# Optimization experiments

Hardware: AMD Instinct MI355X
Metric: run time of the kernel (lower is better)

Reference implementation:

```python
import jax, jax.numpy as jnp
import numpy as np

ALPHA = 0.9     # projection strength
EPS = 1e-3      # Lyapunov positive-definite regularizer (lyapunov_eps)
B, D, H = 32768, 512, 64


def setup_inputs() -> dict:
    key = jax.random.key(0)
    ks = jax.random.split(key, 8)
    def w(k, shape, fan_in):
        return jax.random.normal(k, shape, jnp.float32) * (1.0 / fan_in) ** 0.5
    return dict(
        x=jax.random.normal(ks[0], (B, D), jnp.float32),
        # dynamics MLP f(x): D -> 64 -> 64 -> D
        W1=w(ks[1], (D, H), D), b1=jnp.zeros((H,), jnp.float32),
        W2=w(ks[2], (H, H), H), b2=jnp.zeros((H,), jnp.float32),
        W3=w(ks[3], (H, D), H), b3=jnp.zeros((D,), jnp.float32),
        # Lyapunov MLP V(z): D -> 64 -> 64 -> 1 (+ eps*||z||^2)
        V1=w(ks[4], (D, H), D), c1=jnp.zeros((H,), jnp.float32),
        V2=w(ks[5], (H, H), H), c2=jnp.zeros((H,), jnp.float32),
        V3=w(ks[6], (H, 1), H), c3=jnp.zeros((1,), jnp.float32),
    )


def reference(x, W1, b1, W2, b2, W3, b3, V1, c1, V2, c2, V3, c3):
    def fnet(xx):  # nominal dynamics: [B,D] -> [B,D]
        h = jax.nn.relu(xx @ W1 + b1)
        h = jax.nn.relu(h @ W2 + b2)
        return h @ W3 + b3

    def vnet(z):  # Lyapunov candidate: [B,D] -> [B]
        h = jax.nn.relu(z @ V1 + c1)
        h = jax.nn.relu(h @ V2 + c2)
        return (h @ V3 + c3)[..., 0] + EPS * jnp.sum(z * z, axis=-1)

    def lyap_sum(xx):
        v = vnet(fnet(xx))
        return jnp.sum(v), v

    # grad_v replicates the in-forward lyapunov.backward(...): dV(f(x))/dx, shape [B,D]
    (_, lyap), grad_v = jax.value_and_grad(lyap_sum, has_aux=True)(x)

    f = fnet(x)                                   # [B, D]
    dot = jnp.sum(grad_v * grad_v, axis=-1)       # bmm(gv, fv): per-sample <grad_v, grad_v>
    denom = jnp.sum(grad_v * grad_v)              # global .pow(2).sum() over all elements
    orth = jax.nn.relu(dot + ALPHA * lyap) / denom  # [B]
    return f - orth[:, None] * grad_v             # diag_embed(orth) @ grad_v
```

## Files before the change

kernel.cpp:

```cpp
#include <hip/hip_runtime.h>

#define ALPHA_C 0.9f
#define EPS_C 1e-3f

typedef unsigned short u16;
typedef __attribute__((ext_vector_type(8))) short short8;
typedef __attribute__((ext_vector_type(4))) float f32x4;
#define MFMA(a, b, c) __builtin_amdgcn_mfma_f32_16x16x32_bf16(a, b, c, 0, 0, 0)

__device__ __forceinline__ u16 f2bf(float f) {
  union { float f; unsigned u; } v; v.f = f;
  unsigned u = v.u;
  u += 0x7FFFu + ((u >> 16) & 1u);
  return (u16)(u >> 16);
}
__device__ __forceinline__ float bf2f(u16 h) {
  union { unsigned u; float f; } v; v.u = ((unsigned)h) << 16;
  return v.f;
}

__global__ __launch_bounds__(256) void k_conv(
    const float* __restrict__ W1, const float* __restrict__ W2, const float* __restrict__ W3,
    const float* __restrict__ V1, const float* __restrict__ V2,
    u16* __restrict__ W1T, u16* __restrict__ W1n, u16* __restrict__ W2T, u16* __restrict__ W2n,
    u16* __restrict__ W3T, u16* __restrict__ W3n, u16* __restrict__ V1T, u16* __restrict__ V1n,
    u16* __restrict__ V2T, u16* __restrict__ V2n) {
  int i = blockIdx.x * 256 + threadIdx.x;
  { float v = W1[i]; int k = i >> 6, j = i & 63; u16 b = f2bf(v); W1n[i] = b; W1T[j * 512 + k] = b; }
  { float v = V1[i]; int k = i >> 6, j = i & 63; u16 b = f2bf(v); V1n[i] = b; V1T[j * 512 + k] = b; }
  { float v = W3[i]; int k = i >> 9, n = i & 511; u16 b = f2bf(v); W3n[i] = b; W3T[n * 64 + k] = b; }
  if (i < 4096) {
    { float v = W2[i]; int k = i >> 6, j = i & 63; u16 b = f2bf(v); W2n[i] = b; W2T[j * 64 + k] = b; }
    { float v = V2[i]; int k = i >> 6, j = i & 63; u16 b = f2bf(v); V2n[i] = b; V2T[j * 64 + k] = b; }
  }
}

__global__ __launch_bounds__(256) void k_h12(
    const float* __restrict__ x, const u16* __restrict__ W1T, const float* __restrict__ b1,
    const u16* __restrict__ W2T, const float* __restrict__ b2,
    u16* __restrict__ H1b, u16* __restrict__ H2b) {
  __shared__ u16 As[64 * 136];
  __shared__ u16 Bs[64 * 136];
  __shared__ u16 W2s[64 * 72];
  __shared__ u16 Hs[64 * 72];
  const int tid = threadIdx.x;
  const int lane = tid & 63, w = tid >> 6, q = lane >> 4, r = lane & 15;
  const int m0 = blockIdx.x * 64;

  #pragma unroll
  for (int c = 0; c < 2; ++c) {
    int idx = c * 256 + tid; int a = idx >> 3, k8 = (idx & 7) * 8;
    *(short8*)&W2s[a * 72 + k8] = *(const short8*)&W2T[a * 64 + k8];
  }

  f32x4 acc[4] = {};
  for (int kc = 0; kc < 4; ++kc) {
    __syncthreads();
    #pragma unroll
    for (int c = 0; c < 8; ++c) {
      int idx = c * 256 + tid; int rr = idx >> 5, k4 = (idx & 31) * 4;
      float4 v = *(const float4*)&x[(size_t)(m0 + rr) * 512 + kc * 128 + k4];
      As[rr * 136 + k4 + 0] = f2bf(v.x);
      As[rr * 136 + k4 + 1] = f2bf(v.y);
      As[rr * 136 + k4 + 2] = f2bf(v.z);
      As[rr * 136 + k4 + 3] = f2bf(v.w);
    }
    #pragma unroll
    for (int c = 0; c < 4; ++c) {
      int idx = c * 256 + tid; int rr = idx >> 4, k8 = (idx & 15) * 8;
      *(short8*)&Bs[rr * 136 + k8] = *(const short8*)&W1T[rr * 512 + kc * 128 + k8];
    }
    __syncthreads();
    #pragma unroll
    for (int ks = 0; ks < 4; ++ks) {
      short8 a = *(const short8*)&As[(w * 16 + r) * 136 + ks * 32 + q * 8];
      #pragma unroll
      for (int t = 0; t < 4; ++t) {
        short8 b = *(const short8*)&Bs[(t * 16 + r) * 136 + ks * 32 + q * 8];
        acc[t] = MFMA(a, b, acc[t]);
      }
    }
  }
  __syncthreads();
  #pragma unroll
  for (int t = 0; t < 4; ++t) {
    int col = t * 16 + r; float bv = b1[col];
    #pragma unroll
    for (int g = 0; g < 4; ++g) {
      float h = acc[t][g] + bv; h = h > 0.f ? h : 0.f;
      Hs[(w * 16 + q * 4 + g) * 72 + col] = f2bf(h);
    }
  }
  __syncthreads();
  #pragma unroll
  for (int c = 0; c < 2; ++c) {
    int idx = c * 256 + tid; int rr = idx >> 3, k8 = (idx & 7) * 8;
    *(short8*)&H1b[(size_t)(m0 + rr) * 64 + k8] = *(const short8*)&Hs[rr * 72 + k8];
  }
  f32x4 acc2[4] = {};
  #pragma unroll
  for (int ks = 0; ks < 2; ++ks) {
    short8 a = *(const short8*)&Hs[(w * 16 + r) * 72 + ks * 32 + q * 8];
    #pragma unroll
    for (int t = 0; t < 4; ++t) {
      short8 b = *(const short8*)&W2s[(t * 16 + r) * 72 + ks * 32 + q * 8];
      acc2[t] = MFMA(a, b, acc2[t]);
    }
  }
  __syncthreads();
  #pragma unroll
  for (int t = 0; t < 4; ++t) {
    int col = t * 16 + r; float bv = b2[col];
    #pragma unroll
    for (int g = 0; g < 4; ++g) {
      float h = acc2[t][g] + bv; h = h > 0.f ? h : 0.f;
      Hs[(w * 16 + q * 4 + g) * 72 + col] = f2bf(h);
    }
  }
  __syncthreads();
  #pragma unroll
  for (int c = 0; c < 2; ++c) {
    int idx = c * 256 + tid; int rr = idx >> 3, k8 = (idx & 7) * 8;
    *(short8*)&H2b[(size_t)(m0 + rr) * 64 + k8] = *(const short8*)&Hs[rr * 72 + k8];
  }
}

__global__ __launch_bounds__(256) void k_fg1s(
    const u16* __restrict__ H2b, const u16* __restrict__ W3T, const float* __restrict__ b3,
    const u16* __restrict__ V1T, const float* __restrict__ c1,
    const u16* __restrict__ V2Tb, const u16* __restrict__ V2nb, const float* __restrict__ c2,
    const float* __restrict__ V3, const float* __restrict__ c3,
    u16* __restrict__ Fb, u16* __restrict__ S2b, float* __restrict__ LYAP) {
  __shared__ u16 H2s[64 * 72];
  __shared__ u16 Bs[128 * 72];
  __shared__ u16 As[64 * 136];
  const int tid = threadIdx.x;
  const int lane = tid & 63, w = tid >> 6, q = lane >> 4, r = lane & 15;
  const int m0 = blockIdx.x * 64;

  #pragma unroll
  for (int c = 0; c < 2; ++c) {
    int idx = c * 256 + tid; int a = idx >> 3, k8 = (idx & 7) * 8;
    *(short8*)&H2s[a * 72 + k8] = *(const short8*)&H2b[(size_t)(m0 + a) * 64 + k8];
  }
  f32x4 g1acc[4] = {};
  float ssq[4] = {0.f, 0.f, 0.f, 0.f};
  for (int nc = 0; nc < 4; ++nc) {
    __syncthreads();
    #pragma unroll
    for (int c = 0; c < 4; ++c) {
      int idx = c * 256 + tid; int nl = idx >> 3, k8 = (idx & 7) * 8;
      *(short8*)&Bs[nl * 72 + k8] = *(const short8*)&W3T[(size_t)(nc * 128 + nl) * 64 + k8];
    }
    __syncthreads();
    f32x4 facc[8] = {};
    #pragma unroll
    for (int ks = 0; ks < 2; ++ks) {
      short8 a = *(const short8*)&H2s[(w * 16 + r) * 72 + ks * 32 + q * 8];
      #pragma unroll
      for (int t = 0; t < 8; ++t) {
        short8 b = *(const short8*)&Bs[(t * 16 + r) * 72 + ks * 32 + q * 8];
        facc[t] = MFMA(a, b, facc[t]);
      }
    }
    #pragma unroll
    for (int t = 0; t < 8; ++t) {
      int colg = nc * 128 + t * 16 + r;
      float bv = b3[colg];
      #pragma unroll
      for (int g = 0; g < 4; ++g) {
        float v = facc[t][g] + bv;
        ssq[g] += v * v;
        As[(w * 16 + q * 4 + g) * 136 + t * 16 + r] = f2bf(v);
      }
    }
    __syncthreads();
    #pragma unroll
    for (int c = 0; c < 4; ++c) {
      int idx = c * 256 + tid; int jj = idx >> 4, k8 = (idx & 15) * 8;
      *(short8*)&Bs[jj * 136 + k8] = *(const short8*)&V1T[(size_t)jj * 512 + nc * 128 + k8];
    }
    __syncthreads();
    #pragma unroll
    for (int ks = 0; ks < 4; ++ks) {
      short8 a = *(const short8*)&As[(w * 16 + r) * 136 + ks * 32 + q * 8];
      #pragma unroll
      for (int t = 0; t < 4; ++t) {
        short8 b = *(const short8*)&Bs[(t * 16 + r) * 136 + ks * 32 + q * 8];
        g1acc[t] = MFMA(a, b, g1acc[t]);
      }
    }
    #pragma unroll
    for (int c = 0; c < 4; ++c) {
      int idx = c * 256 + tid; int rr = idx >> 4, k8 = (idx & 15) * 8;
      *(short8*)&Fb[(size_t)(m0 + rr) * 512 + nc * 128 + k8] = *(const short8*)&As[rr * 136 + k8];
    }
  }
  __syncthreads();
  f32x4 g1v[4];
  #pragma unroll
  for (int t = 0; t < 4; ++t) {
    int col = t * 16 + r; float cv = c1[col];
    #pragma unroll
    for (int g = 0; g < 4; ++g) {
      float v = g1acc[t][g] + cv; v = v > 0.f ? v : 0.f;
      g1v[t][g] = v;
      H2s[(w * 16 + q * 4 + g) * 72 + col] = f2bf(v);
    }
  }
  #pragma unroll
  for (int c = 0; c < 2; ++c) {
    int idx = c * 256 + tid; int a = idx >> 3, k8 = (idx & 7) * 8;
    *(short8*)&Bs[a * 72 + k8] = *(const short8*)&V2Tb[a * 64 + k8];
  }
  __syncthreads();
  f32x4 g2acc[4] = {};
  #pragma unroll
  for (int ks = 0; ks < 2; ++ks) {
    short8 a = *(const short8*)&H2s[(w * 16 + r) * 72 + ks * 32 + q * 8];
    #pragma unroll
    for (int t = 0; t < 4; ++t) {
      short8 b = *(const short8*)&Bs[(t * 16 + r) * 72 + ks * 32 + q * 8];
      g2acc[t] = MFMA(a, b, g2acc[t]);
    }
  }
  __syncthreads();
  float tot[4] = {0.f, 0.f, 0.f, 0.f};
  #pragma unroll
  for (int t = 0; t < 4; ++t) {
    int col = t * 16 + r;
    float c2v = c2[col], v3v = V3[col];
    #pragma unroll
    for (int g = 0; g < 4; ++g) {
      float pre = g2acc[t][g] + c2v;
      float g2 = pre > 0.f ? pre : 0.f;
      float s3 = pre > 0.f ? v3v : 0.f;
      H2s[(w * 16 + q * 4 + g) * 72 + col] = f2bf(s3);
      tot[g] += g2 * v3v;
    }
  }
  #pragma unroll
  for (int c = 0; c < 2; ++c) {
    int idx = c * 256 + tid; int a = idx >> 3, k8 = (idx & 7) * 8;
    *(short8*)&Bs[a * 72 + k8] = *(const short8*)&V2nb[a * 64 + k8];
  }
  __syncthreads();
  f32x4 s2acc[4] = {};
  #pragma unroll
  for (int ks = 0; ks < 2; ++ks) {
    short8 a = *(const short8*)&H2s[(w * 16 + r) * 72 + ks * 32 + q * 8];
    #pragma unroll
    for (int t = 0; t < 4; ++t) {
      short8 b = *(const short8*)&Bs[(t * 16 + r) * 72 + ks * 32 + q * 8];
      s2acc[t] = MFMA(a, b, s2acc[t]);
    }
  }
  #pragma unroll
  for (int t = 0; t < 4; ++t) {
    int col = t * 16 + r;
    #pragma unroll
    for (int g = 0; g < 4; ++g) {
      float sv = g1v[t][g] > 0.f ? s2acc[t][g] : 0.f;
      S2b[(size_t)(m0 + w * 16 + q * 4 + g) * 64 + col] = f2bf(sv);
    }
  }
  float c3v = c3[0];
  #pragma unroll
  for (int g = 0; g < 4; ++g) {
    float s = tot[g] + EPS_C * ssq[g];
    s += __shfl_xor(s, 1); s += __shfl_xor(s, 2); s += __shfl_xor(s, 4); s += __shfl_xor(s, 8);
    if (r == 0) LYAP[m0 + w * 16 + q * 4 + g] = s + c3v;
  }
}

__global__ __launch_bounds__(256) void k_utg(
    const u16* __restrict__ S2b, const u16* __restrict__ V1n, const u16* __restrict__ Fb,
    const u16* __restrict__ W3n, const u16* __restrict__ W2n, const u16* __restrict__ W1n,
    const u16* __restrict__ H1b, const u16* __restrict__ H2b,
    const float* __restrict__ LYAP,
    u16* __restrict__ T2b, float* __restrict__ NUM, float* __restrict__ DP) {
  __shared__ u16 S2s[64 * 72];
  __shared__ u16 Bs[128 * 72];
  __shared__ u16 As[64 * 136];
  __shared__ u16 W2s[64 * 72];
  __shared__ u16 T3s[64 * 72];
  __shared__ float dred[4];
  const int tid = threadIdx.x;
  const int lane = tid & 63, w = tid >> 6, q = lane >> 4, r = lane & 15;
  const int m0 = blockIdx.x * 64;

  #pragma unroll
  for (int c = 0; c < 2; ++c) {
    int idx = c * 256 + tid; int a = idx >> 3, k8 = (idx & 7) * 8;
    *(short8*)&S2s[a * 72 + k8] = *(const short8*)&S2b[(size_t)(m0 + a) * 64 + k8];
    *(short8*)&W2s[a * 72 + k8] = *(const short8*)&W2n[a * 64 + k8];
  }
  f32x4 t3acc[4] = {};
  for (int nc = 0; nc < 4; ++nc) {
    __syncthreads();
    #pragma unroll
    for (int c = 0; c < 4; ++c) {
      int idx = c * 256 + tid; int rr = idx >> 4, k8 = (idx & 15) * 8;
      *(short8*)&As[rr * 136 + k8] = *(const short8*)&Fb[(size_t)(m0 + rr) * 512 + nc * 128 + k8];
    }
    #pragma unroll
    for (int c = 0; c < 4; ++c) {
      int idx = c * 256 + tid; int nl = idx >> 3, k8 = (idx & 7) * 8;
      *(short8*)&Bs[nl * 72 + k8] = *(const short8*)&V1n[(size_t)(nc * 128 + nl) * 64 + k8];
    }
    __syncthreads();
    f32x4 uacc[8] = {};
    #pragma unroll
    for (int ks = 0; ks < 2; ++ks) {
      short8 a = *(const short8*)&S2s[(w * 16 + r) * 72 + ks * 32 + q * 8];
      #pragma unroll
      for (int t = 0; t < 8; ++t) {
        short8 b = *(const short8*)&Bs[(t * 16 + r) * 72 + ks * 32 + q * 8];
        uacc[t] = MFMA(a, b, uacc[t]);
      }
    }
    #pragma unroll
    for (int t = 0; t < 8; ++t) {
      #pragma unroll
      for (int g = 0; g < 4; ++g) {
        int addr = (w * 16 + q * 4 + g) * 136 + t * 16 + r;
        As[addr] = f2bf(uacc[t][g] + 2.f * EPS_C * bf2f(As[addr]));
      }
    }
    __syncthreads();
    #pragma unroll
    for (int c = 0; c < 4; ++c) {
      int idx = c * 256 + tid; int jj = idx >> 4, k8 = (idx & 15) * 8;
      *(short8*)&Bs[jj * 136 + k8] = *(const short8*)&W3n[(size_t)jj * 512 + nc * 128 + k8];
    }
    __syncthreads();
    #pragma unroll
    for (int ks = 0; ks < 4; ++ks) {
      short8 a = *(const short8*)&As[(w * 16 + r) * 136 + ks * 32 + q * 8];
      #pragma unroll
      for (int t = 0; t < 4; ++t) {
        short8 b = *(const short8*)&Bs[(t * 16 + r) * 136 + ks * 32 + q * 8];
        t3acc[t] = MFMA(a, b, t3acc[t]);
      }
    }
  }
  #pragma unroll
  for (int t = 0; t < 4; ++t) {
    int col = t * 16 + r;
    #pragma unroll
    for (int g = 0; g < 4; ++g) {
      int rl = w * 16 + q * 4 + g;
      u16 h2u = H2b[(size_t)(m0 + rl) * 64 + col];
      float v = h2u ? t3acc[t][g] : 0.f;
      T3s[rl * 72 + col] = f2bf(v);
    }
  }
  f32x4 t2acc[4] = {};
  #pragma unroll
  for (int ks = 0; ks < 2; ++ks) {
    short8 a = *(const short8*)&T3s[(w * 16 + r) * 72 + ks * 32 + q * 8];
    #pragma unroll
    for (int t = 0; t < 4; ++t) {
      short8 b = *(const short8*)&W2s[(t * 16 + r) * 72 + ks * 32 + q * 8];
      t2acc[t] = MFMA(a, b, t2acc[t]);
    }
  }
  __syncthreads();
  #pragma unroll
  for (int t = 0; t < 4; ++t) {
    int col = t * 16 + r;
    #pragma unroll
    for (int g = 0; g < 4; ++g) {
      int rl = w * 16 + q * 4 + g;
      u16 h1u = H1b[(size_t)(m0 + rl) * 64 + col];
      u16 tv = h1u ? f2bf(t2acc[t][g]) : 0;
      T2b[(size_t)(m0 + rl) * 64 + col] = tv;
      S2s[rl * 72 + col] = tv;
    }
  }
  float ssq[4] = {0.f, 0.f, 0.f, 0.f};
  for (int nc = 0; nc < 4; ++nc) {
    __syncthreads();
    #pragma unroll
    for (int c = 0; c < 4; ++c) {
      int idx = c * 256 + tid; int nl = idx >> 3, k8 = (idx & 7) * 8;
      *(short8*)&Bs[nl * 72 + k8] = *(const short8*)&W1n[(size_t)(nc * 128 + nl) * 64 + k8];
    }
    __syncthreads();
    f32x4 acc[8] = {};
    #pragma unroll
    for (int ks = 0; ks < 2; ++ks) {
      short8 a = *(const short8*)&S2s[(w * 16 + r) * 72 + ks * 32 + q * 8];
      #pragma unroll
      for (int t = 0; t < 8; ++t) {
        short8 b = *(const short8*)&Bs[(t * 16 + r) * 72 + ks * 32 + q * 8];
        acc[t] = MFMA(a, b, acc[t]);
      }
    }
    #pragma unroll
    for (int t = 0; t < 8; ++t)
      #pragma unroll
      for (int g = 0; g < 4; ++g) ssq[g] += acc[t][g] * acc[t][g];
  }
  float totw = 0.f;
  #pragma unroll
  for (int g = 0; g < 4; ++g) {
    float s = ssq[g];
    s += __shfl_xor(s, 1); s += __shfl_xor(s, 2); s += __shfl_xor(s, 4); s += __shfl_xor(s, 8);
    if (r == 0) {
      int rowg = m0 + w * 16 + q * 4 + g;
      float nm = s + ALPHA_C * LYAP[rowg];
      NUM[rowg] = nm > 0.f ? nm : 0.f;
    }
    s += __shfl_xor(s, 16); s += __shfl_xor(s, 32);
    totw += s;
  }
  if (lane == 0) dred[w] = totw;
  __syncthreads();
  if (tid == 0) atomicAdd(&DP[blockIdx.x & 255], dred[0] + dred[1] + dred[2] + dred[3]);
}

__global__ __launch_bounds__(256) void k_out(
    const u16* __restrict__ T2b, const u16* __restrict__ W1n,
    const u16* __restrict__ Fb, const float* __restrict__ NUM, const float* __restrict__ DP,
    float* __restrict__ out) {
  __shared__ u16 T2s[64 * 72];
  __shared__ u16 Bs[128 * 72];
  __shared__ u16 As[64 * 136];
  __shared__ float red[256];
  const int tid = threadIdx.x;
  const int lane = tid & 63, w = tid >> 6, q = lane >> 4, r = lane & 15;
  const int m0 = blockIdx.x * 64;
  red[tid] = DP[tid];
  #pragma unroll
  for (int c = 0; c < 2; ++c) {
    int idx = c * 256 + tid; int a = idx >> 3, k8 = (idx & 7) * 8;
    *(short8*)&T2s[a * 72 + k8] = *(const short8*)&T2b[(size_t)(m0 + a) * 64 + k8];
  }
  __syncthreads();
  for (int s = 128; s >= 1; s >>= 1) {
    if (tid < s) red[tid] += red[tid + s];
    __syncthreads();
  }
  const float inv_denom = 1.f / red[0];
  float sc[4];
  #pragma unroll
  for (int g = 0; g < 4; ++g) sc[g] = NUM[m0 + w * 16 + q * 4 + g] * inv_denom;
  for (int nc = 0; nc < 4; ++nc) {
    __syncthreads();
    #pragma unroll
    for (int c = 0; c < 4; ++c) {
      int idx = c * 256 + tid; int nl = idx >> 3, k8 = (idx & 7) * 8;
      *(short8*)&Bs[nl * 72 + k8] = *(const short8*)&W1n[(size_t)(nc * 128 + nl) * 64 + k8];
    }
    #pragma unroll
    for (int c = 0; c < 4; ++c) {
      int idx = c * 256 + tid; int rr = idx >> 4, k8 = (idx & 15) * 8;
      *(short8*)&As[rr * 136 + k8] = *(const short8*)&Fb[(size_t)(m0 + rr) * 512 + nc * 128 + k8];
    }
    __syncthreads();
    f32x4 acc[8] = {};
    #pragma unroll
    for (int ks = 0; ks < 2; ++ks) {
      short8 a = *(const short8*)&T2s[(w * 16 + r) * 72 + ks * 32 + q * 8];
      #pragma unroll
      for (int t = 0; t < 8; ++t) {
        short8 b = *(const short8*)&Bs[(t * 16 + r) * 72 + ks * 32 + q * 8];
        acc[t] = MFMA(a, b, acc[t]);
      }
    }
    #pragma unroll
    for (int t = 0; t < 8; ++t) {
      int colg = nc * 128 + t * 16 + r;
      #pragma unroll
      for (int g = 0; g < 4; ++g) {
        int rl = w * 16 + q * 4 + g;
        float fv = bf2f(As[rl * 136 + t * 16 + r]);
        out[(size_t)(m0 + rl) * 512 + colg] = fv - sc[g] * acc[t][g];
      }
    }
  }
}

extern "C" void kernel_launch(void* const* d_in, const int* in_sizes, int n_in,
                              void* d_out, int out_size, void* d_ws, size_t ws_size,
                              hipStream_t stream) {
  const float* x  = (const float*)d_in[0];
  const float* W1 = (const float*)d_in[1];
  const float* b1 = (const float*)d_in[2];
  const float* W2 = (const float*)d_in[3];
  const float* b2 = (const float*)d_in[4];
  const float* W3 = (const float*)d_in[5];
  const float* b3 = (const float*)d_in[6];
  const float* V1 = (const float*)d_in[7];
  const float* c1 = (const float*)d_in[8];
  const float* V2 = (const float*)d_in[9];
  const float* c2 = (const float*)d_in[10];
  const float* V3 = (const float*)d_in[11];
  const float* c3 = (const float*)d_in[12];
  float* out = (float*)d_out;

  u16* Fb = (u16*)d_ws;
  float* LYAP = (float*)(Fb + 16777216);
  float* NUM  = LYAP + 32768;
  float* DP   = NUM + 32768;
  u16* H1b  = (u16*)(DP + 256);
  u16* H2b  = H1b + 2097152;
  u16* S2b  = H2b + 2097152;
  u16* T2b  = S2b + 2097152;
  u16* W1Tb = T2b + 2097152;
  u16* W1nb = W1Tb + 32768;
  u16* W2Tb = W1nb + 32768;
  u16* W2nb = W2Tb + 4096;
  u16* W3Tb = W2nb + 4096;
  u16* W3nb = W3Tb + 32768;
  u16* V1Tb = W3nb + 32768;
  u16* V1nb = V1Tb + 32768;
  u16* V2Tb = V1nb + 32768;
  u16* V2nb = V2Tb + 4096;

  hipMemsetAsync(DP, 0, 256 * sizeof(float), stream);

  k_conv<<<128, 256, 0, stream>>>(W1, W2, W3, V1, V2,
                                  W1Tb, W1nb, W2Tb, W2nb, W3Tb, W3nb, V1Tb, V1nb, V2Tb, V2nb);
  k_h12<<<512, 256, 0, stream>>>(x, W1Tb, b1, W2Tb, b2, H1b, H2b);
  k_fg1s<<<512, 256, 0, stream>>>(H2b, W3Tb, b3, V1Tb, c1, V2Tb, V2nb, c2, V3, c3, Fb, S2b, LYAP);
  k_utg<<<512, 256, 0, stream>>>(S2b, V1nb, Fb, W3nb, W2nb, W1nb, H1b, H2b, LYAP, T2b, NUM, DP);
  k_out<<<512, 256, 0, stream>>>(T2b, W1nb, Fb, NUM, DP, out);
}
```

Baseline: 201.6 us.

## Fuse forward and backward MLP kernels into one per-tile kernel, drop block syncs

```diff
diff --git a/kernel.cpp b/kernel.cpp
--- a/kernel.cpp
+++ b/kernel.cpp
@@ -7,6 +7,7 @@
 typedef __attribute__((ext_vector_type(8))) short short8;
 typedef __attribute__((ext_vector_type(4))) float f32x4;
 #define MFMA(a, b, c) __builtin_amdgcn_mfma_f32_16x16x32_bf16(a, b, c, 0, 0, 0)
+#define LDS_FENCE() asm volatile("" ::: "memory")
 
 __device__ __forceinline__ u16 f2bf(float f) {
   union { float f; unsigned u; } v; v.f = f;
@@ -35,287 +36,192 @@
   }
 }
 
-__global__ __launch_bounds__(256) void k_h12(
-    const float* __restrict__ x, const u16* __restrict__ W1T, const float* __restrict__ b1,
+__global__ __launch_bounds__(256) void k_fused(
+    const float* __restrict__ x,
+    const u16* __restrict__ W1T, const float* __restrict__ b1,
     const u16* __restrict__ W2T, const float* __restrict__ b2,
-    u16* __restrict__ H1b, u16* __restrict__ H2b) {
+    const u16* __restrict__ W3T, const float* __restrict__ b3,
+    const u16* __restrict__ V1T, const float* __restrict__ c1,
+    const u16* __restrict__ V2T, const u16* __restrict__ V2n, const float* __restrict__ c2,
+    const float* __restrict__ V3, const float* __restrict__ c3,
+    const u16* __restrict__ V1n, const u16* __restrict__ W3n,
+    const u16* __restrict__ W2n, const u16* __restrict__ W1n,
+    u16* __restrict__ Fb, u16* __restrict__ T2b,
+    float* __restrict__ NUM, float* __restrict__ DP) {
+  __shared__ u16 H1s[64 * 72];
+  __shared__ u16 H2s[64 * 72];
+  __shared__ u16 S2s[64 * 72];
   __shared__ u16 As[64 * 136];
-  __shared__ u16 Bs[64 * 136];
-  __shared__ u16 W2s[64 * 72];
-  __shared__ u16 Hs[64 * 72];
-  const int tid = threadIdx.x;
-  const int lane = tid & 63, w = tid >> 6, q = lane >> 4, r = lane & 15;
-  const int m0 = blockIdx.x * 64;
-
-  #pragma unroll
-  for (int c = 0; c < 2; ++c) {
-    int idx = c * 256 + tid; int a = idx >> 3, k8 = (idx & 7) * 8;
-    *(short8*)&W2s[a * 72 + k8] = *(const short8*)&W2T[a * 64 + k8];
-  }
-
-  f32x4 acc[4] = {};
-  for (int kc = 0; kc < 4; ++kc) {
-    __syncthreads();
-    #pragma unroll
-    for (int c = 0; c < 8; ++c) {
-      int idx = c * 256 + tid; int rr = idx >> 5, k4 = (idx & 31) * 4;
-      float4 v = *(const float4*)&x[(size_t)(m0 + rr) * 512 + kc * 128 + k4];
-      As[rr * 136 + k4 + 0] = f2bf(v.x);
-      As[rr * 136 + k4 + 1] = f2bf(v.y);
-      As[rr * 136 + k4 + 2] = f2bf(v.z);
-      As[rr * 136 + k4 + 3] = f2bf(v.w);
-    }
-    #pragma unroll
-    for (int c = 0; c < 4; ++c) {
-      int idx = c * 256 + tid; int rr = idx >> 4, k8 = (idx & 15) * 8;
-      *(short8*)&Bs[rr * 136 + k8] = *(const short8*)&W1T[rr * 512 + kc * 128 + k8];
-    }
-    __syncthreads();
-    #pragma unroll
-    for (int ks = 0; ks < 4; ++ks) {
-      short8 a = *(const short8*)&As[(w * 16 + r) * 136 + ks * 32 + q * 8];
-      #pragma unroll
-      for (int t = 0; t < 4; ++t) {
-        short8 b = *(const short8*)&Bs[(t * 16 + r) * 136 + ks * 32 + q * 8];
-        acc[t] = MFMA(a, b, acc[t]);
-      }
-    }
-  }
-  __syncthreads();
-  #pragma unroll
-  for (int t = 0; t < 4; ++t) {
-    int col = t * 16 + r; float bv = b1[col];
-    #pragma unroll
-    for (int g = 0; g < 4; ++g) {
-      float h = acc[t][g] + bv; h = h > 0.f ? h : 0.f;
-      Hs[(w * 16 + q * 4 + g) * 72 + col] = f2bf(h);
-    }
-  }
-  __syncthreads();
-  #pragma unroll
-  for (int c = 0; c < 2; ++c) {
-    int idx = c * 256 + tid; int rr = idx >> 3, k8 = (idx & 7) * 8;
-    *(short8*)&H1b[(size_t)(m0 + rr) * 64 + k8] = *(const short8*)&Hs[rr * 72 + k8];
-  }
-  f32x4 acc2[4] = {};
-  #pragma unroll
-  for (int ks = 0; ks < 2; ++ks) {
-    short8 a = *(const short8*)&Hs[(w * 16 + r) * 72 + ks * 32 + q * 8];
-    #pragma unroll
-    for (int t = 0; t < 4; ++t) {
-      short8 b = *(const short8*)&W2s[(t * 16 + r) * 72 + ks * 32 + q * 8];
-      acc2[t] = MFMA(a, b, acc2[t]);
-    }
-  }
-  __syncthreads();
-  #pragma unroll
-  for (int t = 0; t < 4; ++t) {
-    int col = t * 16 + r; float bv = b2[col];
-    #pragma unroll
-    for (int g = 0; g < 4; ++g) {
-      float h = acc2[t][g] + bv; h = h > 0.f ? h : 0.f;
-      Hs[(w * 16 + q * 4 + g) * 72 + col] = f2bf(h);
-    }
-  }
-  __syncthreads();
-  #pragma unroll
-  for (int c = 0; c < 2; ++c) {
-    int idx = c * 256 + tid; int rr = idx >> 3, k8 = (idx & 7) * 8;
-    *(short8*)&H2b[(size_t)(m0 + rr) * 64 + k8] = *(const short8*)&Hs[rr * 72 + k8];
-  }
-}
-
-__global__ __launch_bounds__(256) void k_fg1s(
-    const u16* __restrict__ H2b, const u16* __restrict__ W3T, const float* __restrict__ b3,
-    const u16* __restrict__ V1T, const float* __restrict__ c1,
-    const u16* __restrict__ V2Tb, const u16* __restrict__ V2nb, const float* __restrict__ c2,
-    const float* __restrict__ V3, const float* __restrict__ c3,
-    u16* __restrict__ Fb, u16* __restrict__ S2b, float* __restrict__ LYAP) {
-  __shared__ u16 H2s[64 * 72];
-  __shared__ u16 Bs[128 * 72];
-  __shared__ u16 As[64 * 136];
-  const int tid = threadIdx.x;
-  const int lane = tid & 63, w = tid >> 6, q = lane >> 4, r = lane & 15;
-  const int m0 = blockIdx.x * 64;
-
-  #pragma unroll
-  for (int c = 0; c < 2; ++c) {
-    int idx = c * 256 + tid; int a = idx >> 3, k8 = (idx & 7) * 8;
-    *(short8*)&H2s[a * 72 + k8] = *(const short8*)&H2b[(size_t)(m0 + a) * 64 + k8];
-  }
-  f32x4 g1acc[4] = {};
-  float ssq[4] = {0.f, 0.f, 0.f, 0.f};
-  for (int nc = 0; nc < 4; ++nc) {
-    __syncthreads();
-    #pragma unroll
-    for (int c = 0; c < 4; ++c) {
-      int idx = c * 256 + tid; int nl = idx >> 3, k8 = (idx & 7) * 8;
-      *(short8*)&Bs[nl * 72 + k8] = *(const short8*)&W3T[(size_t)(nc * 128 + nl) * 64 + k8];
-    }
-    __syncthreads();
-    f32x4 facc[8] = {};
-    #pragma unroll
-    for (int ks = 0; ks < 2; ++ks) {
-      short8 a = *(const short8*)&H2s[(w * 16 + r) * 72 + ks * 32 + q * 8];
-      #pragma unroll
-      for (int t = 0; t < 8; ++t) {
-        short8 b = *(const short8*)&Bs[(t * 16 + r) * 72 + ks * 32 + q * 8];
-        facc[t] = MFMA(a, b, facc[t]);
-      }
-    }
-    #pragma unroll
-    for (int t = 0; t < 8; ++t) {
-      int colg = nc * 128 + t * 16 + r;
-      float bv = b3[colg];
-      #pragma unroll
-      for (int g = 0; g < 4; ++g) {
-        float v = facc[t][g] + bv;
-        ssq[g] += v * v;
-        As[(w * 16 + q * 4 + g) * 136 + t * 16 + r] = f2bf(v);
-      }
-    }
-    __syncthreads();
-    #pragma unroll
-    for (int c = 0; c < 4; ++c) {
-      int idx = c * 256 + tid; int jj = idx >> 4, k8 = (idx & 15) * 8;
-      *(short8*)&Bs[jj * 136 + k8] = *(const short8*)&V1T[(size_t)jj * 512 + nc * 128 + k8];
-    }
-    __syncthreads();
-    #pragma unroll
-    for (int ks = 0; ks < 4; ++ks) {
-      short8 a = *(const short8*)&As[(w * 16 + r) * 136 + ks * 32 + q * 8];
-      #pragma unroll
-      for (int t = 0; t < 4; ++t) {
-        short8 b = *(const short8*)&Bs[(t * 16 + r) * 136 + ks * 32 + q * 8];
-        g1acc[t] = MFMA(a, b, g1acc[t]);
-      }
-    }
-    #pragma unroll
-    for (int c = 0; c < 4; ++c) {
-      int idx = c * 256 + tid; int rr = idx >> 4, k8 = (idx & 15) * 8;
-      *(short8*)&Fb[(size_t)(m0 + rr) * 512 + nc * 128 + k8] = *(const short8*)&As[rr * 136 + k8];
-    }
-  }
-  __syncthreads();
-  f32x4 g1v[4];
-  #pragma unroll
-  for (int t = 0; t < 4; ++t) {
-    int col = t * 16 + r; float cv = c1[col];
-    #pragma unroll
-    for (int g = 0; g < 4; ++g) {
-      float v = g1acc[t][g] + cv; v = v > 0.f ? v : 0.f;
-      g1v[t][g] = v;
-      H2s[(w * 16 + q * 4 + g) * 72 + col] = f2bf(v);
-    }
-  }
-  #pragma unroll
-  for (int c = 0; c < 2; ++c) {
-    int idx = c * 256 + tid; int a = idx >> 3, k8 = (idx & 7) * 8;
-    *(short8*)&Bs[a * 72 + k8] = *(const short8*)&V2Tb[a * 64 + k8];
-  }
-  __syncthreads();
-  f32x4 g2acc[4] = {};
-  #pragma unroll
-  for (int ks = 0; ks < 2; ++ks) {
-    short8 a = *(const short8*)&H2s[(w * 16 + r) * 72 + ks * 32 + q * 8];
-    #pragma unroll
-    for (int t = 0; t < 4; ++t) {
-      short8 b = *(const short8*)&Bs[(t * 16 + r) * 72 + ks * 32 + q * 8];
-      g2acc[t] = MFMA(a, b, g2acc[t]);
-    }
-  }
-  __syncthreads();
-  float tot[4] = {0.f, 0.f, 0.f, 0.f};
-  #pragma unroll
-  for (int t = 0; t < 4; ++t) {
-    int col = t * 16 + r;
-    float c2v = c2[col], v3v = V3[col];
-    #pragma unroll
-    for (int g = 0; g < 4; ++g) {
-      float pre = g2acc[t][g] + c2v;
-      float g2 = pre > 0.f ? pre : 0.f;
-      float s3 = pre > 0.f ? v3v : 0.f;
-      H2s[(w * 16 + q * 4 + g) * 72 + col] = f2bf(s3);
-      tot[g] += g2 * v3v;
-    }
-  }
-  #pragma unroll
-  for (int c = 0; c < 2; ++c) {
-    int idx = c * 256 + tid; int a = idx >> 3, k8 = (idx & 7) * 8;
-    *(short8*)&Bs[a * 72 + k8] = *(const short8*)&V2nb[a * 64 + k8];
-  }
-  __syncthreads();
-  f32x4 s2acc[4] = {};
-  #pragma unroll
-  for (int ks = 0; ks < 2; ++ks) {
-    short8 a = *(const short8*)&H2s[(w * 16 + r) * 72 + ks * 32 + q * 8];
-    #pragma unroll
-    for (int t = 0; t < 4; ++t) {
-      short8 b = *(const short8*)&Bs[(t * 16 + r) * 72 + ks * 32 + q * 8];
-      s2acc[t] = MFMA(a, b, s2acc[t]);
-    }
-  }
-  #pragma unroll
-  for (int t = 0; t < 4; ++t) {
-    int col = t * 16 + r;
-    #pragma unroll
-    for (int g = 0; g < 4; ++g) {
-      float sv = g1v[t][g] > 0.f ? s2acc[t][g] : 0.f;
-      S2b[(size_t)(m0 + w * 16 + q * 4 + g) * 64 + col] = f2bf(sv);
-    }
-  }
-  float c3v = c3[0];
-  #pragma unroll
-  for (int g = 0; g < 4; ++g) {
-    float s = tot[g] + EPS_C * ssq[g];
-    s += __shfl_xor(s, 1); s += __shfl_xor(s, 2); s += __shfl_xor(s, 4); s += __shfl_xor(s, 8);
-    if (r == 0) LYAP[m0 + w * 16 + q * 4 + g] = s + c3v;
-  }
-}
-
-__global__ __launch_bounds__(256) void k_utg(
-    const u16* __restrict__ S2b, const u16* __restrict__ V1n, const u16* __restrict__ Fb,
-    const u16* __restrict__ W3n, const u16* __restrict__ W2n, const u16* __restrict__ W1n,
-    const u16* __restrict__ H1b, const u16* __restrict__ H2b,
-    const float* __restrict__ LYAP,
-    u16* __restrict__ T2b, float* __restrict__ NUM, float* __restrict__ DP) {
-  __shared__ u16 S2s[64 * 72];
-  __shared__ u16 Bs[128 * 72];
-  __shared__ u16 As[64 * 136];
-  __shared__ u16 W2s[64 * 72];
-  __shared__ u16 T3s[64 * 72];
   __shared__ float dred[4];
   const int tid = threadIdx.x;
   const int lane = tid & 63, w = tid >> 6, q = lane >> 4, r = lane & 15;
   const int m0 = blockIdx.x * 64;
-
-  #pragma unroll
-  for (int c = 0; c < 2; ++c) {
-    int idx = c * 256 + tid; int a = idx >> 3, k8 = (idx & 7) * 8;
-    *(short8*)&S2s[a * 72 + k8] = *(const short8*)&S2b[(size_t)(m0 + a) * 64 + k8];
-    *(short8*)&W2s[a * 72 + k8] = *(const short8*)&W2n[a * 64 + k8];
-  }
+  const int arow = w * 16 + r;
+
+  f32x4 acc1[4] = {};
+  #pragma unroll 4
+  for (int ks = 0; ks < 16; ++ks) {
+    const float4 v0 = *(const float4*)&x[(size_t)(m0 + arow) * 512 + ks * 32 + q * 8];
+    const float4 v1 = *(const float4*)&x[(size_t)(m0 + arow) * 512 + ks * 32 + q * 8 + 4];
+    short8 a;
+    a[0] = (short)f2bf(v0.x); a[1] = (short)f2bf(v0.y);
+    a[2] = (short)f2bf(v0.z); a[3] = (short)f2bf(v0.w);
+    a[4] = (short)f2bf(v1.x); a[5] = (short)f2bf(v1.y);
+    a[6] = (short)f2bf(v1.z); a[7] = (short)f2bf(v1.w);
+    #pragma unroll
+    for (int t = 0; t < 4; ++t) {
+      short8 b = *(const short8*)&W1T[(t * 16 + r) * 512 + ks * 32 + q * 8];
+      acc1[t] = MFMA(a, b, acc1[t]);
+    }
+  }
+  #pragma unroll
+  for (int t = 0; t < 4; ++t) {
+    int col = t * 16 + r; float bv = b1[col];
+    #pragma unroll
+    for (int g = 0; g < 4; ++g) {
+      float h = acc1[t][g] + bv; h = h > 0.f ? h : 0.f;
+      H1s[(w * 16 + q * 4 + g) * 72 + col] = f2bf(h);
+    }
+  }
+  LDS_FENCE();
+
+  f32x4 acc2[4] = {};
+  #pragma unroll
+  for (int ks = 0; ks < 2; ++ks) {
+    short8 a = *(const short8*)&H1s[arow * 72 + ks * 32 + q * 8];
+    #pragma unroll
+    for (int t = 0; t < 4; ++t) {
+      short8 b = *(const short8*)&W2T[(t * 16 + r) * 64 + ks * 32 + q * 8];
+      acc2[t] = MFMA(a, b, acc2[t]);
+    }
+  }
+  #pragma unroll
+  for (int t = 0; t < 4; ++t) {
+    int col = t * 16 + r; float bv = b2[col];
+    #pragma unroll
+    for (int g = 0; g < 4; ++g) {
+      float h = acc2[t][g] + bv; h = h > 0.f ? h : 0.f;
+      H2s[(w * 16 + q * 4 + g) * 72 + col] = f2bf(h);
+    }
+  }
+  LDS_FENCE();
+
+  f32x4 g1acc[4] = {};
+  float ssq[4] = {0.f, 0.f, 0.f, 0.f};
+  #pragma unroll 1
+  for (int nc = 0; nc < 4; ++nc) {
+    f32x4 facc[8] = {};
+    #pragma unroll
+    for (int ks = 0; ks < 2; ++ks) {
+      short8 a = *(const short8*)&H2s[arow * 72 + ks * 32 + q * 8];
+      #pragma unroll
+      for (int t = 0; t < 8; ++t) {
+        short8 b = *(const short8*)&W3T[(nc * 128 + t * 16 + r) * 64 + ks * 32 + q * 8];
+        facc[t] = MFMA(a, b, facc[t]);
+      }
+    }
+    #pragma unroll
+    for (int t = 0; t < 8; ++t) {
+      int colg = nc * 128 + t * 16 + r;
+      float bv = b3[colg];
+      #pragma unroll
+      for (int g = 0; g < 4; ++g) {
+        float v = facc[t][g] + bv;
+        ssq[g] += v * v;
+        u16 bb = f2bf(v);
+        As[(w * 16 + q * 4 + g) * 136 + t * 16 + r] = bb;
+        Fb[(size_t)(m0 + w * 16 + q * 4 + g) * 512 + colg] = bb;
+      }
+    }
+    LDS_FENCE();
+    #pragma unroll
+    for (int ks = 0; ks < 4; ++ks) {
+      short8 a = *(const short8*)&As[arow * 136 + ks * 32 + q * 8];
+      #pragma unroll
+      for (int t = 0; t < 4; ++t) {
+        short8 b = *(const short8*)&V1T[(t * 16 + r) * 512 + nc * 128 + ks * 32 + q * 8];
+        g1acc[t] = MFMA(a, b, g1acc[t]);
+      }
+    }
+  }
+
+  f32x4 g1v[4];
+  #pragma unroll
+  for (int t = 0; t < 4; ++t) {
+    int col = t * 16 + r; float cv = c1[col];
+    #pragma unroll
+    for (int g = 0; g < 4; ++g) {
+      float v = g1acc[t][g] + cv; v = v > 0.f ? v : 0.f;
+      g1v[t][g] = v;
+      S2s[(w * 16 + q * 4 + g) * 72 + col] = f2bf(v);
+    }
+  }
+  LDS_FENCE();
+  f32x4 g2acc[4] = {};
+  #pragma unroll
+  for (int ks = 0; ks < 2; ++ks) {
+    short8 a = *(const short8*)&S2s[arow * 72 + ks * 32 + q * 8];
+    #pragma unroll
+    for (int t = 0; t < 4; ++t) {
+      short8 b = *(const short8*)&V2T[(t * 16 + r) * 64 + ks * 32 + q * 8];
+      g2acc[t] = MFMA(a, b, g2acc[t]);
+    }
+  }
+  float tot[4] = {0.f, 0.f, 0.f, 0.f};
+  #pragma unroll
+  for (int t = 0; t < 4; ++t) {
+    int col = t * 16 + r;
+    float c2v = c2[col], v3v = V3[col];
+    #pragma unroll
+    for (int g = 0; g < 4; ++g) {
+      float pre = g2acc[t][g] + c2v;
+      float g2 = pre > 0.f ? pre : 0.f;
+      S2s[(w * 16 + q * 4 + g) * 72 + col] = pre > 0.f ? f2bf(v3v) : (u16)0;
+      tot[g] += g2 * v3v;
+    }
+  }
+  LDS_FENCE();
+  f32x4 s2acc[4] = {};
+  #pragma unroll
+  for (int ks = 0; ks < 2; ++ks) {
+    short8 a = *(const short8*)&S2s[arow * 72 + ks * 32 + q * 8];
+    #pragma unroll
+    for (int t = 0; t < 4; ++t) {
+      short8 b = *(const short8*)&V2n[(t * 16 + r) * 64 + ks * 32 + q * 8];
+      s2acc[t] = MFMA(a, b, s2acc[t]);
+    }
+  }
+  #pragma unroll
+  for (int t = 0; t < 4; ++t) {
+    int col = t * 16 + r;
+    #pragma unroll
+    for (int g = 0; g < 4; ++g) {
+      float sv = g1v[t][g] > 0.f ? s2acc[t][g] : 0.f;
+      S2s[(w * 16 + q * 4 + g) * 72 + col] = f2bf(sv);
+    }
+  }
+  LDS_FENCE();
+  float c3v = c3[0];
+  float lyap_row[4];
+  #pragma unroll
+  for (int g = 0; g < 4; ++g) {
+    float s = tot[g] + EPS_C * ssq[g];
+    s += __shfl_xor(s, 1); s += __shfl_xor(s, 2); s += __shfl_xor(s, 4); s += __shfl_xor(s, 8);
+    lyap_row[g] = s + c3v;
+  }
+
+  asm volatile("s_waitcnt vmcnt(0)" ::: "memory");
+
   f32x4 t3acc[4] = {};
+  #pragma unroll 1
   for (int nc = 0; nc < 4; ++nc) {
-    __syncthreads();
-    #pragma unroll
-    for (int c = 0; c < 4; ++c) {
-      int idx = c * 256 + tid; int rr = idx >> 4, k8 = (idx & 15) * 8;
-      *(short8*)&As[rr * 136 + k8] = *(const short8*)&Fb[(size_t)(m0 + rr) * 512 + nc * 128 + k8];
-    }
-    #pragma unroll
-    for (int c = 0; c < 4; ++c) {
-      int idx = c * 256 + tid; int nl = idx >> 3, k8 = (idx & 7) * 8;
-      *(short8*)&Bs[nl * 72 + k8] = *(const short8*)&V1n[(size_t)(nc * 128 + nl) * 64 + k8];
-    }
-    __syncthreads();
     f32x4 uacc[8] = {};
     #pragma unroll
     for (int ks = 0; ks < 2; ++ks) {
-      short8 a = *(const short8*)&S2s[(w * 16 + r) * 72 + ks * 32 + q * 8];
+      short8 a = *(const short8*)&S2s[arow * 72 + ks * 32 + q * 8];
       #pragma unroll
       for (int t = 0; t < 8; ++t) {
-        short8 b = *(const short8*)&Bs[(t * 16 + r) * 72 + ks * 32 + q * 8];
+        short8 b = *(const short8*)&V1n[(nc * 128 + t * 16 + r) * 64 + ks * 32 + q * 8];
         uacc[t] = MFMA(a, b, uacc[t]);
       }
     }
@@ -323,23 +229,18 @@
     for (int t = 0; t < 8; ++t) {
       #pragma unroll
       for (int g = 0; g < 4; ++g) {
-        int addr = (w * 16 + q * 4 + g) * 136 + t * 16 + r;
-        As[addr] = f2bf(uacc[t][g] + 2.f * EPS_C * bf2f(As[addr]));
-      }
-    }
-    __syncthreads();
-    #pragma unroll
-    for (int c = 0; c < 4; ++c) {
-      int idx = c * 256 + tid; int jj = idx >> 4, k8 = (idx & 15) * 8;
-      *(short8*)&Bs[jj * 136 + k8] = *(const short8*)&W3n[(size_t)jj * 512 + nc * 128 + k8];
-    }
-    __syncthreads();
+        int rl = w * 16 + q * 4 + g;
+        float f = bf2f(Fb[(size_t)(m0 + rl) * 512 + nc * 128 + t * 16 + r]);
+        As[rl * 136 + t * 16 + r] = f2bf(uacc[t][g] + 2.f * EPS_C * f);
+      }
+    }
+    LDS_FENCE();
     #pragma unroll
     for (int ks = 0; ks < 4; ++ks) {
-      short8 a = *(const short8*)&As[(w * 16 + r) * 136 + ks * 32 + q * 8];
+      short8 a = *(const short8*)&As[arow * 136 + ks * 32 + q * 8];
       #pragma unroll
       for (int t = 0; t < 4; ++t) {
-        short8 b = *(const short8*)&Bs[(t * 16 + r) * 136 + ks * 32 + q * 8];
+        short8 b = *(const short8*)&W3n[(size_t)(t * 16 + r) * 512 + nc * 128 + ks * 32 + q * 8];
         t3acc[t] = MFMA(a, b, t3acc[t]);
       }
     }
@@ -349,67 +250,62 @@
     int col = t * 16 + r;
     #pragma unroll
     for (int g = 0; g < 4; ++g) {
+      int addr = (w * 16 + q * 4 + g) * 72 + col;
+      u16 h2 = H2s[addr];
+      H2s[addr] = h2 ? f2bf(t3acc[t][g]) : (u16)0;
+    }
+  }
+  LDS_FENCE();
+  f32x4 t2acc[4] = {};
+  #pragma unroll
+  for (int ks = 0; ks < 2; ++ks) {
+    short8 a = *(const short8*)&H2s[arow * 72 + ks * 32 + q * 8];
+    #pragma unroll
+    for (int t = 0; t < 4; ++t) {
+      short8 b = *(const short8*)&W2n[(t * 16 + r) * 64 + ks * 32 + q * 8];
+      t2acc[t] = MFMA(a, b, t2acc[t]);
+    }
+  }
+  #pragma unroll
+  for (int t = 0; t < 4; ++t) {
+    int col = t * 16 + r;
+    #pragma unroll
+    for (int g = 0; g < 4; ++g) {
       int rl = w * 16 + q * 4 + g;
-      u16 h2u = H2b[(size_t)(m0 + rl) * 64 + col];
-      float v = h2u ? t3acc[t][g] : 0.f;
-      T3s[rl * 72 + col] = f2bf(v);
-    }
-  }
-  f32x4 t2acc[4] = {};
-  #pragma unroll
-  for (int ks = 0; ks < 2; ++ks) {
-    short8 a = *(const short8*)&T3s[(w * 16 + r) * 72 + ks * 32 + q * 8];
-    #pragma unroll
-    for (int t = 0; t < 4; ++t) {
-      short8 b = *(const short8*)&W2s[(t * 16 + r) * 72 + ks * 32 + q * 8];
-      t2acc[t] = MFMA(a, b, t2acc[t]);
-    }
-  }
-  __syncthreads();
-  #pragma unroll
-  for (int t = 0; t < 4; ++t) {
-    int col = t * 16 + r;
-    #pragma unroll
-    for (int g = 0; g < 4; ++g) {
-      int rl = w * 16 + q * 4 + g;
-      u16 h1u = H1b[(size_t)(m0 + rl) * 64 + col];
-      u16 tv = h1u ? f2bf(t2acc[t][g]) : 0;
+      int addr = rl * 72 + col;
+      u16 h1 = H1s[addr];
+      u16 tv = h1 ? f2bf(t2acc[t][g]) : (u16)0;
+      H1s[addr] = tv;
       T2b[(size_t)(m0 + rl) * 64 + col] = tv;
-      S2s[rl * 72 + col] = tv;
-    }
-  }
-  float ssq[4] = {0.f, 0.f, 0.f, 0.f};
+    }
+  }
+  LDS_FENCE();
+  float ssq2[4] = {0.f, 0.f, 0.f, 0.f};
+  #pragma unroll 1
   for (int nc = 0; nc < 4; ++nc) {
-    __syncthreads();
-    #pragma unroll
-    for (int c = 0; c < 4; ++c) {
-      int idx = c * 256 + tid; int nl = idx >> 3, k8 = (idx & 7) * 8;
-      *(short8*)&Bs[nl * 72 + k8] = *(const short8*)&W1n[(size_t)(nc * 128 + nl) * 64 + k8];
-    }
-    __syncthreads();
     f32x4 acc[8] = {};
     #pragma unroll
     for (int ks = 0; ks < 2; ++ks) {
-      short8 a = *(const short8*)&S2s[(w * 16 + r) * 72 + ks * 32 + q * 8];
+      short8 a = *(const short8*)&H1s[arow * 72 + ks * 32 + q * 8];
       #pragma unroll
       for (int t = 0; t < 8; ++t) {
-        short8 b = *(const short8*)&Bs[(t * 16 + r) * 72 + ks * 32 + q * 8];
+        short8 b = *(const short8*)&W1n[(nc * 128 + t * 16 + r) * 64 + ks * 32 + q * 8];
         acc[t] = MFMA(a, b, acc[t]);
       }
     }
     #pragma unroll
     for (int t = 0; t < 8; ++t)
       #pragma unroll
-      for (int g = 0; g < 4; ++g) ssq[g] += acc[t][g] * acc[t][g];
+      for (int g = 0; g < 4; ++g) ssq2[g] += acc[t][g] * acc[t][g];
   }
   float totw = 0.f;
   #pragma unroll
   for (int g = 0; g < 4; ++g) {
-    float s = ssq[g];
+    float s = ssq2[g];
     s += __shfl_xor(s, 1); s += __shfl_xor(s, 2); s += __shfl_xor(s, 4); s += __shfl_xor(s, 8);
     if (r == 0) {
       int rowg = m0 + w * 16 + q * 4 + g;
-      float nm = s + ALPHA_C * LYAP[rowg];
+      float nm = s + ALPHA_C * lyap_row[g];
       NUM[rowg] = nm > 0.f ? nm : 0.f;
     }
     s += __shfl_xor(s, 16); s += __shfl_xor(s, 32);
@@ -424,19 +320,12 @@
     const u16* __restrict__ T2b, const u16* __restrict__ W1n,
     const u16* __restrict__ Fb, const float* __restrict__ NUM, const float* __restrict__ DP,
     float* __restrict__ out) {
-  __shared__ u16 T2s[64 * 72];
-  __shared__ u16 Bs[128 * 72];
-  __shared__ u16 As[64 * 136];
   __shared__ float red[256];
   const int tid = threadIdx.x;
   const int lane = tid & 63, w = tid >> 6, q = lane >> 4, r = lane & 15;
   const int m0 = blockIdx.x * 64;
+  const int arow = w * 16 + r;
   red[tid] = DP[tid];
-  #pragma unroll
-  for (int c = 0; c < 2; ++c) {
-    int idx = c * 256 + tid; int a = idx >> 3, k8 = (idx & 7) * 8;
-    *(short8*)&T2s[a * 72 + k8] = *(const short8*)&T2b[(size_t)(m0 + a) * 64 + k8];
-  }
   __syncthreads();
   for (int s = 128; s >= 1; s >>= 1) {
     if (tid < s) red[tid] += red[tid + s];
@@ -446,28 +335,17 @@
   float sc[4];
   #pragma unroll
   for (int g = 0; g < 4; ++g) sc[g] = NUM[m0 + w * 16 + q * 4 + g] * inv_denom;
+  short8 a0 = *(const short8*)&T2b[(size_t)(m0 + arow) * 64 + q * 8];
+  short8 a1 = *(const short8*)&T2b[(size_t)(m0 + arow) * 64 + 32 + q * 8];
+  #pragma unroll 1
   for (int nc = 0; nc < 4; ++nc) {
-    __syncthreads();
-    #pragma unroll
-    for (int c = 0; c < 4; ++c) {
-      int idx = c * 256 + tid; int nl = idx >> 3, k8 = (idx & 7) * 8;
-      *(short8*)&Bs[nl * 72 + k8] = *(const short8*)&W1n[(size_t)(nc * 128 + nl) * 64 + k8];
-    }
-    #pragma unroll
-    for (int c = 0; c < 4; ++c) {
-      int idx = c * 256 + tid; int rr = idx >> 4, k8 = (idx & 15) * 8;
-      *(short8*)&As[rr * 136 + k8] = *(const short8*)&Fb[(size_t)(m0 + rr) * 512 + nc * 128 + k8];
-    }
-    __syncthreads();
     f32x4 acc[8] = {};
     #pragma unroll
-    for (int ks = 0; ks < 2; ++ks) {
-      short8 a = *(const short8*)&T2s[(w * 16 + r) * 72 + ks * 32 + q * 8];
-      #pragma unroll
-      for (int t = 0; t < 8; ++t) {
-        short8 b = *(const short8*)&Bs[(t * 16 + r) * 72 + ks * 32 + q * 8];
-        acc[t] = MFMA(a, b, acc[t]);
-      }
+    for (int t = 0; t < 8; ++t) {
+      short8 b0 = *(const short8*)&W1n[(nc * 128 + t * 16 + r) * 64 + q * 8];
+      short8 b1 = *(const short8*)&W1n[(nc * 128 + t * 16 + r) * 64 + 32 + q * 8];
+      acc[t] = MFMA(a0, b0, acc[t]);
+      acc[t] = MFMA(a1, b1, acc[t]);
     }
     #pragma unroll
     for (int t = 0; t < 8; ++t) {
@@ -475,7 +353,7 @@
       #pragma unroll
       for (int g = 0; g < 4; ++g) {
         int rl = w * 16 + q * 4 + g;
-        float fv = bf2f(As[rl * 136 + t * 16 + r]);
+        float fv = bf2f(Fb[(size_t)(m0 + rl) * 512 + colg]);
         out[(size_t)(m0 + rl) * 512 + colg] = fv - sc[g] * acc[t][g];
       }
     }
@@ -501,13 +379,9 @@
   float* out = (float*)d_out;
 
   u16* Fb = (u16*)d_ws;
-  float* LYAP = (float*)(Fb + 16777216);
-  float* NUM  = LYAP + 32768;
+  float* NUM  = (float*)(Fb + 16777216);
   float* DP   = NUM + 32768;
-  u16* H1b  = (u16*)(DP + 256);
-  u16* H2b  = H1b + 2097152;
-  u16* S2b  = H2b + 2097152;
-  u16* T2b  = S2b + 2097152;
+  u16* T2b  = (u16*)(DP + 256);
   u16* W1Tb = T2b + 2097152;
   u16* W1nb = W1Tb + 32768;
   u16* W2Tb = W1nb + 32768;
@@ -523,8 +397,8 @@
 
   k_conv<<<128, 256, 0, stream>>>(W1, W2, W3, V1, V2,
                                   W1Tb, W1nb, W2Tb, W2nb, W3Tb, W3nb, V1Tb, V1nb, V2Tb, V2nb);
-  k_h12<<<512, 256, 0, stream>>>(x, W1Tb, b1, W2Tb, b2, H1b, H2b);
-  k_fg1s<<<512, 256, 0, stream>>>(H2b, W3Tb, b3, V1Tb, c1, V2Tb, V2nb, c2, V3, c3, Fb, S2b, LYAP);
-  k_utg<<<512, 256, 0, stream>>>(S2b, V1nb, Fb, W3nb, W2nb, W1nb, H1b, H2b, LYAP, T2b, NUM, DP);
+  k_fused<<<512, 256, 0, stream>>>(x, W1Tb, b1, W2Tb, b2, W3Tb, b3, V1Tb, c1,
+                                   V2Tb, V2nb, c2, V3, c3, V1nb, W3nb, W2nb, W1nb,
+                                   Fb, T2b, NUM, DP);
   k_out<<<512, 256, 0, stream>>>(T2b, W1nb, Fb, NUM, DP, out);
 }
```

After: 280.2 us. 1.39x slower.
